# Performance work log

Hardware: AMD Instinct MI355X
Metric: run time of the kernel (lower is better)

The kernel has to match this reference:

```python
import jax, jax.numpy as jnp
import numpy as np
from jax import lax

B, X, H, W, C = 4, 32, 8, 128, 32  # batch, frames, height, width, channels (dim)


def setup_inputs() -> dict:
    key = jax.random.key(0)
    k1, k2, k3, k4, k5, k6 = jax.random.split(key, 6)
    return {
        "storage": jax.random.normal(k1, (B, X, H, W, C), jnp.float32),
        "target": jax.random.normal(k2, (B, 1, H, W, C), jnp.float32),
        # Conv3d(dim, 2*dim, kernel=(3,1,1), padding=(1,0,0)) weight/bias
        "w_cross": jax.random.normal(k3, (2 * C, C, 3, 1, 1), jnp.float32) * 0.05,
        "b_cross": jax.random.normal(k4, (2 * C,), jnp.float32) * 0.05,
        # Conv2d(dim, dim, kernel=1) weight (stored as [out, in]) / bias
        "w_q": jax.random.normal(k5, (C, C), jnp.float32) * 0.1,
        "b_q": jax.random.normal(k6, (C,), jnp.float32) * 0.1,
    }


def reference(storage, target, w_cross, b_cross, w_q, b_q):
    # storage [B,X,H,W,C] -> transpose(4,1).transpose(4,2) -> [B,C,X,W,H]
    s = jnp.transpose(storage, (0, 4, 1, 3, 2))
    # target [B,1,H,W,C] -> transpose(4,2) -> [B,1,C,W,H] -> squeeze(1) -> [B,C,W,H]
    t = jnp.transpose(target, (0, 1, 4, 3, 2))[:, 0]

    # Conv3d over the X (depth) axis, kernel (3,1,1), padding (1,0,0)
    out = lax.conv_general_dilated(
        s, w_cross, window_strides=(1, 1, 1),
        padding=((1, 1), (0, 0), (0, 0)),
        dimension_numbers=("NCDHW", "OIDHW", "NCDHW"),
    ) + b_cross[None, :, None, None, None]          # [B,2C,X,W,H]
    s_v, s_k = jnp.split(out, 2, axis=1)            # each [B,C,X,W,H]

    # 1x1 Conv2d query projection
    t_q = jnp.einsum("oc,bcwh->bowh", w_q, t) + b_q[None, :, None, None]  # [B,C,W,H]
    # unsqueeze(1).transpose(2,1).repeat over X -> [B,C,X,W,H]
    t_q = jnp.broadcast_to(t_q[:, :, None], (B, C, X, W, H))

    # Faithful torch .view on contiguous [B,C,X,W,H]: row-major reshape mixes C into last dim
    t_q = t_q.reshape(B, X * W, C * H)
    s_v = s_v.reshape(B, X * W, C * H)
    s_k = jnp.swapaxes(s_k.reshape(B, X * W, C * H), 1, 2)  # [B, C*H, X*W]

    kq = jax.nn.softmax(jnp.einsum("bnc,bcm->bnm", t_q, s_k), axis=-1)  # [B, XW, XW]
    final = jnp.einsum("bnm,bmc->bnc", kq, s_v)                          # [B, XW, C*H]
    return final.reshape(B, X, H, W, C)
```

## Files before the change

kernel.cpp:

```cpp
#include <hip/hip_runtime.h>

typedef unsigned short u16;
typedef unsigned int u32;
typedef __attribute__((ext_vector_type(8))) short s16x8;
typedef __attribute__((ext_vector_type(4))) float f32x4;

#define WS_A      0u
#define WS_B      8388608u
#define WS_C      16777216u
#define WS_D      25165824u
#define WS_E      25427968u
#define WS_LP     25452544u
#define WS_NEEDED 25485312u

__device__ __forceinline__ u16 f2bf(float f){
  u32 u = __float_as_uint(f);
  return (u16)((u + 0x7fffu + ((u >> 16) & 1u)) >> 16);
}

__global__ __launch_bounds__(256) void zero_out_kernel(float* __restrict__ out){
  int t = blockIdx.x * 256 + threadIdx.x;
  ((float4*)out)[t] = make_float4(0.f, 0.f, 0.f, 0.f);
}

__global__ __launch_bounds__(256) void prep_kernel(const float* __restrict__ target,
    const float* __restrict__ w_q, const float* __restrict__ b_q, u16* __restrict__ Qbf,
    const float* __restrict__ w_cross, float* __restrict__ wT){
  int bid = blockIdx.x;
  int tid = threadIdx.x;
  if (bid >= 512){
    int t = (bid - 512) * 256 + tid;
    wT[t] = w_cross[(t & 63) * 96 + (t >> 6)];
    return;
  }
  int wc = bid & 3;
  int cq = (bid >> 2) & 31;
  int b  = bid >> 7;
  int wl = tid & 31, h = tid >> 5;
  int w = wc * 32 + wl;
  float in[32];
  const float4* p = (const float4*)(target + (((size_t)b*8 + h)*128 + w)*32);
  #pragma unroll
  for (int q = 0; q < 8; ++q){
    float4 v = p[q];
    in[q*4+0] = v.x; in[q*4+1] = v.y; in[q*4+2] = v.z; in[q*4+3] = v.w;
  }
  float acc = b_q[cq];
  #pragma unroll
  for (int c = 0; c < 32; ++c) acc += in[c] * w_q[cq*32 + c];
  __shared__ float stg[256];
  stg[wl*8 + h] = acc;
  __syncthreads();
  Qbf[((size_t)b*128 + cq*4 + wc)*256 + tid] = f2bf(stg[tid]);
}

__global__ __launch_bounds__(256, 2) void conv_kernel(const float* __restrict__ storage,
    const float* __restrict__ wT, const float* __restrict__ b_cross,
    u16* __restrict__ Kb, u16* __restrict__ Vb){
  int bid = blockIdx.x;
  int wc  = bid & 3;
  int x   = (bid >> 2) & 31;
  int og2 = (bid >> 7) & 3;
  int b   = bid >> 9;
  int tid = threadIdx.x;
  int wl = tid & 31, h = tid >> 5;
  int w = wc * 32 + wl;
  int obase_ch = og2 * 16;

  float acc[16];
  #pragma unroll
  for (int i = 0; i < 16; ++i) acc[i] = b_cross[obase_ch + i];

  #pragma unroll
  for (int dx = 0; dx < 3; ++dx){
    int xx = x + dx - 1;
    if (xx < 0 || xx > 31) continue;
    float vv[32];
    const float4* p = (const float4*)(storage + ((((size_t)b*32 + xx)*8 + h)*128 + w)*32);
    #pragma unroll
    for (int q = 0; q < 8; ++q){
      float4 v = p[q];
      vv[q*4+0] = v.x; vv[q*4+1] = v.y; vv[q*4+2] = v.z; vv[q*4+3] = v.w;
    }
    #pragma unroll
    for (int c = 0; c < 32; ++c){
      float v = vv[c];
      const float* wp = wT + (c*3 + dx)*64 + obase_ch;
      #pragma unroll
      for (int i = 0; i < 16; ++i) acc[i] = fmaf(v, wp[i], acc[i]);
    }
  }

  int m = wl*8 + h;
  size_t base = ((size_t)b*4096 + (size_t)x*4 + wc)*256 + m;
  if (og2 < 2){
    #pragma unroll
    for (int i = 0; i < 16; ++i)
      Vb[base + (size_t)(obase_ch + i)*32768] = f2bf(acc[i]);
  } else {
    #pragma unroll
    for (int i = 0; i < 16; ++i)
      Kb[base + (size_t)(obase_ch + i - 32)*32768] = f2bf(acc[i]);
  }
}

__global__ __launch_bounds__(256, 2) void flash_kernel(const u16* __restrict__ Qbf,
    const u16* __restrict__ Kb, const u16* __restrict__ Vb,
    float* __restrict__ Opart, float* __restrict__ lpart){
  int kq = blockIdx.x & 15, rb = (blockIdx.x >> 4) & 7, b = blockIdx.x >> 7;
  int tid = threadIdx.x;
  int w = tid >> 6, lane = tid & 63, l15 = lane & 15, quad = lane >> 4;

  __shared__ alignas(16) u16 Vts[256 * 64];
  __shared__ alignas(16) u16 Ps[16 * 64];
  __shared__ float lsumW[64];

  s16x8 qa[8];
  {
    const u16* qp = Qbf + ((size_t)(b*128 + rb*16 + l15))*256 + quad*8;
    #pragma unroll
    for (int ks = 0; ks < 8; ++ks) qa[ks] = *(const s16x8*)(qp + ks*32);
  }

  int jl4 = tid & 15, mseg = tid >> 4;
  const u16* kbase = Kb + ((size_t)(b*4096 + kq*256 + w*16 + l15))*256 + quad*8;
  const u16* vbase = Vb + ((size_t)(b*4096 + kq*256 + jl4*4))*256 + mseg*16;

  s16x8 kr[8];
  #pragma unroll
  for (int ks = 0; ks < 8; ++ks) kr[ks] = *(const s16x8*)(kbase + ks*32);
  u32 kv[4][8];
  #pragma unroll
  for (int kk = 0; kk < 4; ++kk){
    uint4 a = *(const uint4*)(vbase + kk*256);
    uint4 b2 = *(const uint4*)(vbase + kk*256 + 8);
    kv[kk][0]=a.x; kv[kk][1]=a.y; kv[kk][2]=a.z; kv[kk][3]=a.w;
    kv[kk][4]=b2.x; kv[kk][5]=b2.y; kv[kk][6]=b2.z; kv[kk][7]=b2.w;
  }

  float lacc[4] = {0.f, 0.f, 0.f, 0.f};
  f32x4 oc[4];
  #pragma unroll
  for (int mt = 0; mt < 4; ++mt) oc[mt] = (f32x4){0.f,0.f,0.f,0.f};

  #pragma unroll
  for (int it = 0; it < 4; ++it){
    if (it > 0) __syncthreads();

    #pragma unroll
    for (int i = 0; i < 16; ++i){
      int d = i >> 1;
      u32 e0, e1, e2, e3;
      if (i & 1){ e0 = kv[0][d] >> 16;     e1 = kv[1][d] >> 16;
                  e2 = kv[2][d] >> 16;     e3 = kv[3][d] >> 16; }
      else      { e0 = kv[0][d] & 0xffffu; e1 = kv[1][d] & 0xffffu;
                  e2 = kv[2][d] & 0xffffu; e3 = kv[3][d] & 0xffffu; }
      int m = mseg*16 + i;
      int col = (((jl4 >> 1) ^ (m & 7)) << 3) + ((jl4 & 1) << 2);
      *(uint2*)&Vts[m*64 + col] = make_uint2(e0 | (e1 << 16), e2 | (e3 << 16));
    }

    f32x4 s0 = {0.f,0.f,0.f,0.f}, s1 = {0.f,0.f,0.f,0.f};
    #pragma unroll
    for (int ks = 0; ks < 8; ks += 2){
      s0 = __builtin_amdgcn_mfma_f32_16x16x32_bf16(qa[ks],   kr[ks],   s0, 0, 0, 0);
      s1 = __builtin_amdgcn_mfma_f32_16x16x32_bf16(qa[ks+1], kr[ks+1], s1, 0, 0, 0);
    }
    int b8k = w*2 + (l15 >> 3);
    #pragma unroll
    for (int reg = 0; reg < 4; ++reg){
      float sv = fminf(s0[reg] + s1[reg], 80.f);
      float p = __expf(sv);
      int row = quad*4 + reg;
      Ps[row*64 + ((b8k ^ (row & 7)) << 3) + (l15 & 7)] = f2bf(p);
      lacc[reg] += p;
    }

    if (it < 3){
      const u16* vp = vbase + (it+1)*16384;
      #pragma unroll
      for (int kk = 0; kk < 4; ++kk){
        uint4 a = *(const uint4*)(vp + kk*256);
        uint4 b2 = *(const uint4*)(vp + kk*256 + 8);
        kv[kk][0]=a.x; kv[kk][1]=a.y; kv[kk][2]=a.z; kv[kk][3]=a.w;
        kv[kk][4]=b2.x; kv[kk][5]=b2.y; kv[kk][6]=b2.z; kv[kk][7]=b2.w;
      }
    }
    __syncthreads();

    if (it < 3){
      const u16* kp = kbase + (it+1)*16384;
      #pragma unroll
      for (int ks = 0; ks < 8; ++ks) kr[ks] = *(const s16x8*)(kp + ks*32);
    }
    #pragma unroll
    for (int ks2 = 0; ks2 < 2; ++ks2){
      int b8 = ks2*4 + quad;
      s16x8 pb = *(const s16x8*)&Ps[l15*64 + ((b8 ^ (l15 & 7)) << 3)];
      #pragma unroll
      for (int mt = 0; mt < 4; ++mt){
        int mrow = (w*4 + mt)*16 + l15;
        s16x8 af = *(const s16x8*)&Vts[mrow*64 + ((b8 ^ (mrow & 7)) << 3)];
        oc[mt] = __builtin_amdgcn_mfma_f32_16x16x32_bf16(af, pb, oc[mt], 0, 0, 0);
      }
    }
  }

  #pragma unroll
  for (int reg = 0; reg < 4; ++reg){
    float t = lacc[reg];
    t += __shfl_xor(t, 1); t += __shfl_xor(t, 2);
    t += __shfl_xor(t, 4); t += __shfl_xor(t, 8);
    lacc[reg] = t;
  }
  if (l15 == 0){
    #pragma unroll
    for (int reg = 0; reg < 4; ++reg) lsumW[w*16 + quad*4 + reg] = lacc[reg];
  }
  __syncthreads();
  if (tid < 16)
    lpart[(b*16 + kq)*128 + rb*16 + tid] =
        lsumW[tid] + lsumW[16 + tid] + lsumW[32 + tid] + lsumW[48 + tid];
  {
    float* dst = Opart + ((size_t)((b*16 + kq)*128 + rb*16 + l15))*256 + w*64 + quad*4;
    #pragma unroll
    for (int mt = 0; mt < 4; ++mt)
      *(float4*)(dst + mt*16) = make_float4(oc[mt][0], oc[mt][1], oc[mt][2], oc[mt][3]);
  }
}

__global__ __launch_bounds__(256) void combine_kernel(const float* __restrict__ lpart,
    const float* __restrict__ Opart, float* __restrict__ out){
  int r = blockIdx.x & 127, b = blockIdx.x >> 7;
  int m = threadIdx.x;
  float L = 0.f, o = 0.f;
  #pragma unroll
  for (int kq = 0; kq < 16; ++kq){
    L += lpart[(b*16 + kq)*128 + r];
    o += Opart[((size_t)((b*16 + kq)*128 + r))*256 + m];
  }
  o /= L;
  int cq = r >> 2, whi = r & 3;
  size_t obase = ((size_t)b*32 + cq) * 32768;
  #pragma unroll
  for (int hh = 0; hh < 8; ++hh){
    #pragma unroll
    for (int wt = 0; wt < 4; ++wt){
      out[obase + hh*4096 + wt*1024 + whi*256 + m] = o;
    }
  }
}

extern "C" void kernel_launch(void* const* d_in, const int* in_sizes, int n_in,
                              void* d_out, int out_size, void* d_ws, size_t ws_size,
                              hipStream_t stream){
  const float* storage = (const float*)d_in[0];
  const float* target  = (const float*)d_in[1];
  const float* w_cross = (const float*)d_in[2];
  const float* b_cross = (const float*)d_in[3];
  const float* w_q     = (const float*)d_in[4];
  const float* b_q     = (const float*)d_in[5];
  float* out = (float*)d_out;

  if (ws_size < (size_t)WS_NEEDED){
    zero_out_kernel<<<dim3(4096), dim3(256), 0, stream>>>(out);
    return;
  }

  char* ws = (char*)d_ws;
  float* Opart = (float*)(ws + WS_A);
  u16*   Kb    = (u16*)(ws + WS_B);
  u16*   Vb    = (u16*)(ws + WS_C);
  u16*   Qbf   = (u16*)(ws + WS_D);
  float* wT    = (float*)(ws + WS_E);
  float* lpart = (float*)(ws + WS_LP);

  prep_kernel    <<<dim3(536),  dim3(256), 0, stream>>>(target, w_q, b_q, Qbf, w_cross, wT);
  conv_kernel    <<<dim3(2048), dim3(256), 0, stream>>>(storage, wT, b_cross, Kb, Vb);
  flash_kernel   <<<dim3(512),  dim3(256), 0, stream>>>(Qbf, Kb, Vb, Opart, lpart);
  combine_kernel <<<dim3(512),  dim3(256), 0, stream>>>(lpart, Opart, out);
}
```

Baseline: 135.5 us.

## Fuse Q projection into flash kernel and drop prep kernel; coalesce conv stores

Removes the separate prep kernel. Each flash block now computes its own 16 rows of the Q projection from target into shared memory, and the conv kernel reads w_cross directly instead of a transposed copy. The conv kernel also stages its bf16 outputs in shared memory so it can write them with coalesced 16-byte stores instead of scattered 2-byte stores. This saves a kernel launch and a global round trip for Q, but each flash block redundantly reads target (16 blocks per row group) and does extra FMAs, and the conv weights are now read with a 96-float stride.

```diff
diff --git a/kernel.cpp b/kernel.cpp
--- a/kernel.cpp
+++ b/kernel.cpp
@@ -8,8 +8,6 @@
 #define WS_A      0u
 #define WS_B      8388608u
 #define WS_C      16777216u
-#define WS_D      25165824u
-#define WS_E      25427968u
 #define WS_LP     25452544u
 #define WS_NEEDED 25485312u
 
@@ -23,39 +21,8 @@
   ((float4*)out)[t] = make_float4(0.f, 0.f, 0.f, 0.f);
 }
 
-__global__ __launch_bounds__(256) void prep_kernel(const float* __restrict__ target,
-    const float* __restrict__ w_q, const float* __restrict__ b_q, u16* __restrict__ Qbf,
-    const float* __restrict__ w_cross, float* __restrict__ wT){
-  int bid = blockIdx.x;
-  int tid = threadIdx.x;
-  if (bid >= 512){
-    int t = (bid - 512) * 256 + tid;
-    wT[t] = w_cross[(t & 63) * 96 + (t >> 6)];
-    return;
-  }
-  int wc = bid & 3;
-  int cq = (bid >> 2) & 31;
-  int b  = bid >> 7;
-  int wl = tid & 31, h = tid >> 5;
-  int w = wc * 32 + wl;
-  float in[32];
-  const float4* p = (const float4*)(target + (((size_t)b*8 + h)*128 + w)*32);
-  #pragma unroll
-  for (int q = 0; q < 8; ++q){
-    float4 v = p[q];
-    in[q*4+0] = v.x; in[q*4+1] = v.y; in[q*4+2] = v.z; in[q*4+3] = v.w;
-  }
-  float acc = b_q[cq];
-  #pragma unroll
-  for (int c = 0; c < 32; ++c) acc += in[c] * w_q[cq*32 + c];
-  __shared__ float stg[256];
-  stg[wl*8 + h] = acc;
-  __syncthreads();
-  Qbf[((size_t)b*128 + cq*4 + wc)*256 + tid] = f2bf(stg[tid]);
-}
-
 __global__ __launch_bounds__(256, 2) void conv_kernel(const float* __restrict__ storage,
-    const float* __restrict__ wT, const float* __restrict__ b_cross,
+    const float* __restrict__ w_cross, const float* __restrict__ b_cross,
     u16* __restrict__ Kb, u16* __restrict__ Vb){
   int bid = blockIdx.x;
   int wc  = bid & 3;
@@ -85,26 +52,27 @@
     #pragma unroll
     for (int c = 0; c < 32; ++c){
       float v = vv[c];
-      const float* wp = wT + (c*3 + dx)*64 + obase_ch;
-      #pragma unroll
-      for (int i = 0; i < 16; ++i) acc[i] = fmaf(v, wp[i], acc[i]);
-    }
-  }
-
+      const float* wp = w_cross + (size_t)obase_ch*96 + (c*3 + dx);
+      #pragma unroll
+      for (int i = 0; i < 16; ++i) acc[i] = fmaf(v, wp[i*96], acc[i]);
+    }
+  }
+
+  __shared__ u16 st[16*256];
   int m = wl*8 + h;
-  size_t base = ((size_t)b*4096 + (size_t)x*4 + wc)*256 + m;
-  if (og2 < 2){
-    #pragma unroll
-    for (int i = 0; i < 16; ++i)
-      Vb[base + (size_t)(obase_ch + i)*32768] = f2bf(acc[i]);
-  } else {
-    #pragma unroll
-    for (int i = 0; i < 16; ++i)
-      Kb[base + (size_t)(obase_ch + i - 32)*32768] = f2bf(acc[i]);
-  }
-}
-
-__global__ __launch_bounds__(256, 2) void flash_kernel(const u16* __restrict__ Qbf,
+  #pragma unroll
+  for (int i = 0; i < 16; ++i) st[i*256 + m] = f2bf(acc[i]);
+  __syncthreads();
+  int ch = tid >> 4, m16 = (tid & 15) * 16;
+  int ck = obase_ch + ch - (og2 >= 2 ? 32 : 0);
+  size_t base = ((size_t)b*4096 + (size_t)x*4 + wc)*256 + (size_t)ck*32768 + m16;
+  u16* dst = (og2 < 2 ? Vb : Kb) + base;
+  *(uint4*)dst       = *(const uint4*)&st[ch*256 + m16];
+  *(uint4*)(dst + 8) = *(const uint4*)&st[ch*256 + m16 + 8];
+}
+
+__global__ __launch_bounds__(256, 2) void flash_kernel(const float* __restrict__ target,
+    const float* __restrict__ w_q, const float* __restrict__ b_q,
     const u16* __restrict__ Kb, const u16* __restrict__ Vb,
     float* __restrict__ Opart, float* __restrict__ lpart){
   int kq = blockIdx.x & 15, rb = (blockIdx.x >> 4) & 7, b = blockIdx.x >> 7;
@@ -115,12 +83,37 @@
   __shared__ alignas(16) u16 Ps[16 * 64];
   __shared__ float lsumW[64];
 
+  u16* stgQ = Vts;
+  {
+    int wl = tid & 31, h = tid >> 5;
+    #pragma unroll
+    for (int wcq = 0; wcq < 4; ++wcq){
+      float in[32];
+      const float4* p = (const float4*)(target + (((size_t)b*8 + h)*128 + wcq*32 + wl)*32);
+      #pragma unroll
+      for (int q = 0; q < 8; ++q){
+        float4 v = p[q];
+        in[q*4+0] = v.x; in[q*4+1] = v.y; in[q*4+2] = v.z; in[q*4+3] = v.w;
+      }
+      #pragma unroll
+      for (int cql = 0; cql < 4; ++cql){
+        int cq = rb*4 + cql;
+        float acc = b_q[cq];
+        #pragma unroll
+        for (int c = 0; c < 32; ++c) acc = fmaf(in[c], w_q[cq*32 + c], acc);
+        stgQ[(cql*4 + wcq)*264 + wl*8 + h] = f2bf(acc);
+      }
+    }
+  }
+  __syncthreads();
+
   s16x8 qa[8];
   {
-    const u16* qp = Qbf + ((size_t)(b*128 + rb*16 + l15))*256 + quad*8;
+    const u16* qp = stgQ + l15*264 + quad*8;
     #pragma unroll
     for (int ks = 0; ks < 8; ++ks) qa[ks] = *(const s16x8*)(qp + ks*32);
   }
+  __syncthreads();
 
   int jl4 = tid & 15, mseg = tid >> 4;
   const u16* kbase = Kb + ((size_t)(b*4096 + kq*256 + w*16 + l15))*256 + quad*8;
@@ -271,12 +264,9 @@
   float* Opart = (float*)(ws + WS_A);
   u16*   Kb    = (u16*)(ws + WS_B);
   u16*   Vb    = (u16*)(ws + WS_C);
-  u16*   Qbf   = (u16*)(ws + WS_D);
-  float* wT    = (float*)(ws + WS_E);
   float* lpart = (float*)(ws + WS_LP);
 
-  prep_kernel    <<<dim3(536),  dim3(256), 0, stream>>>(target, w_q, b_q, Qbf, w_cross, wT);
-  conv_kernel    <<<dim3(2048), dim3(256), 0, stream>>>(storage, wT, b_cross, Kb, Vb);
-  flash_kernel   <<<dim3(512),  dim3(256), 0, stream>>>(Qbf, Kb, Vb, Opart, lpart);
+  conv_kernel    <<<dim3(2048), dim3(256), 0, stream>>>(storage, w_cross, b_cross, Kb, Vb);
+  flash_kernel   <<<dim3(512),  dim3(256), 0, stream>>>(target, w_q, b_q, Kb, Vb, Opart, lpart);
   combine_kernel <<<dim3(512),  dim3(256), 0, stream>>>(lpart, Opart, out);
 }
```

Result: slower. 154.8 us (+14.2%).
